# Kernel optimization log

Measured on AMD Instinct MI355X. Metric: run time of the kernel, lower is better.

Reference implementation:

```python
import jax, jax.numpy as jnp
import numpy as np

BITS = 4
IN_F = 4096
OUT_F = 4096
NUMVALS = 200000
TOPX = 10
B, S = 4, 2048


def setup_inputs() -> dict:
    key = jax.random.key(0)
    ks = jax.random.split(key, 9)
    x = jax.random.normal(ks[0], (B, S, IN_F), dtype=jnp.float32)
    qweight = jax.random.randint(ks[1], (IN_F // 32 * BITS, OUT_F),
                                 jnp.iinfo(jnp.int32).min, jnp.iinfo(jnp.int32).max,
                                 dtype=jnp.int32)
    lookup_table = jax.random.normal(ks[2], (OUT_F, 2 ** BITS), dtype=jnp.float32) * 0.02
    bias = jax.random.normal(ks[3], (OUT_F,), dtype=jnp.float32) * 0.01
    rows = jnp.sort(jax.random.randint(ks[4], (OUT_F + 1,), 0, NUMVALS, dtype=jnp.int32))
    rows = rows.at[0].set(0).at[-1].set(NUMVALS)  # valid CSR row pointers
    cols = jax.random.randint(ks[5], (NUMVALS,), 0, IN_F, dtype=jnp.int32)
    vals = jax.random.normal(ks[6], (NUMVALS,), dtype=jnp.float32) * 0.02
    full_rows = jax.random.normal(ks[7], (IN_F, TOPX), dtype=jnp.float32) * 0.02
    full_row_indices = (jnp.arange(TOPX, dtype=jnp.int32) * (OUT_F // TOPX))
    return {"x": x, "qweight": qweight, "lookup_table": lookup_table, "bias": bias,
            "rows": rows, "cols": cols, "vals": vals,
            "full_rows": full_rows, "full_row_indices": full_row_indices}


def _dequant(qweight, lookup_table):
    # unpack 4-bit codes packed along infeatures into each int32 word
    per_word = 32 // BITS
    shifts = (jnp.arange(per_word, dtype=jnp.int32) * BITS)
    codes = (qweight[:, None, :] >> shifts[None, :, None]) & ((1 << BITS) - 1)
    codes = codes.reshape(-1, qweight.shape[1])  # (IN_F, OUT_F)
    # per-output-channel LUT gather: W[i, j] = lut[j, codes[i, j]]
    return jnp.take_along_axis(lookup_table.T, codes, axis=0)  # (IN_F, OUT_F)


def reference(x, qweight, lookup_table, bias, rows, cols, vals, full_rows, full_row_indices):
    w = _dequant(qweight, lookup_table)  # (IN_F, OUT_F) float32
    # CSR sparse outlier correction (row pointers over output channels)
    nnz = vals.shape[0]
    row_ids = jnp.searchsorted(rows, jnp.arange(nnz, dtype=jnp.int32), side="right") - 1
    w = w.at[cols, row_ids].add(vals)
    # topX dense outlier channels
    w = w.at[:, full_row_indices].add(full_rows)
    tokens = x.reshape(-1, x.shape[-1])  # (B*S, IN_F)
    y = tokens @ w + bias
    return y.reshape(x.shape[:-1] + (w.shape[1],))
```

## Files before the change

### kernel.cpp

```cpp
#include <hip/hip_runtime.h>
#include <hip/hip_bf16.h>
#include <stdint.h>

#define IN_F 4096
#define OUT_F 4096
#define MTOK 8192
#define TOPX_N 10
#define NUMVALS 200000

typedef __bf16 bf16x8 __attribute__((ext_vector_type(8)));
typedef float f32x4 __attribute__((ext_vector_type(4)));

__device__ __forceinline__ void gld_lds16(const void* g, void* l) {
    __builtin_amdgcn_global_load_lds((const __attribute__((address_space(1))) void*)g,
                                     (__attribute__((address_space(3))) void*)l, 16, 0, 0);
}

__global__ __launch_bounds__(256) void k_dequant(const int* __restrict__ qw,
                                                 const float* __restrict__ lut,
                                                 __bf16* __restrict__ Wt) {
    __shared__ int qs[64 * 65];
    __shared__ float ls[64 * 16];
    const int b = blockIdx.x;
    const int jc = (b & 63) * 64;
    const int wc = (b >> 6) * 64;
    const int t = threadIdx.x;

    {
        float4 v = *(const float4*)(lut + (size_t)(jc + (t >> 2)) * 16 + (t & 3) * 4);
        *(float4*)(ls + (t >> 2) * 16 + (t & 3) * 4) = v;
    }
#pragma unroll
    for (int p = 0; p < 4; ++p) {
        int idx = t + p * 256;
        int row = idx >> 4;
        int c4 = (idx & 15) * 4;
        int4 v = *(const int4*)(qw + (size_t)(wc + row) * OUT_F + jc + c4);
        int base = row * 65 + c4;
        qs[base] = v.x; qs[base + 1] = v.y; qs[base + 2] = v.z; qs[base + 3] = v.w;
    }
    __syncthreads();

    const int wave = t >> 6, lane = t & 63;
#pragma unroll
    for (int i = 0; i < 16; ++i) {
        const int c = wave * 16 + i;
        const unsigned q = (unsigned)qs[lane * 65 + c];
        const float* lp = ls + c * 16;
        bf16x8 v;
#pragma unroll
        for (int e = 0; e < 8; ++e) v[e] = (__bf16)lp[(q >> (4 * e)) & 15];
        *(bf16x8*)(Wt + (size_t)(jc + c) * IN_F + (size_t)(wc + lane) * 8) = v;
    }
}

__global__ __launch_bounds__(256) void k_csr(const int* __restrict__ rows,
                                             const int* __restrict__ cols,
                                             const float* __restrict__ vals,
                                             __bf16* __restrict__ Wt) {
    int n = blockIdx.x * 256 + threadIdx.x;
    if (n >= NUMVALS) return;
    int lo = 0, hi = OUT_F + 1;
    while (lo < hi) {
        int mid = (lo + hi) >> 1;
        if (rows[mid] <= n) lo = mid + 1; else hi = mid;
    }
    int r = lo - 1;
    int c = cols[n];
    float v = vals[n];
    unsigned* wp = (unsigned*)Wt + (((size_t)r * IN_F + c) >> 1);
    unsigned sh = (c & 1) * 16;
    unsigned old = *wp, assumed;
    do {
        assumed = old;
        union { unsigned u; float f; } cv;
        cv.u = ((assumed >> sh) & 0xFFFFu) << 16;
        __bf16 nb = (__bf16)(cv.f + v);
        unsigned nh = *(unsigned short*)&nb;
        unsigned newv = (assumed & ~(0xFFFFu << sh)) | (nh << sh);
        old = atomicCAS(wp, assumed, newv);
    } while (old != assumed);
}

__global__ void k_topx(const float* __restrict__ fr, const int* __restrict__ fri,
                       __bf16* __restrict__ Wt) {
    int i = blockIdx.x * 256 + threadIdx.x;
    if (i >= IN_F) return;
#pragma unroll
    for (int t = 0; t < TOPX_N; ++t) {
        int j = fri[t];
        __bf16* p = Wt + (size_t)j * IN_F + i;
        *p = (__bf16)((float)*p + fr[(size_t)i * TOPX_N + t]);
    }
}

__global__ void k_cvt(const float* __restrict__ x, __bf16* __restrict__ xb) {
    size_t t = (size_t)blockIdx.x * 256 + threadIdx.x;
    const float4* p = (const float4*)x + 2 * t;
    float4 a = p[0], b = p[1];
    bf16x8 v;
    v[0] = (__bf16)a.x; v[1] = (__bf16)a.y; v[2] = (__bf16)a.z; v[3] = (__bf16)a.w;
    v[4] = (__bf16)b.x; v[5] = (__bf16)b.y; v[6] = (__bf16)b.z; v[7] = (__bf16)b.w;
    ((bf16x8*)xb)[t] = v;
}

#define BK_G 32
#define NKT (IN_F / BK_G)
#define TILE_BYTES 16384

__global__ __launch_bounds__(512, 2) void k_gemm(const __bf16* __restrict__ A,
                                                 const __bf16* __restrict__ Bt,
                                                 const float* __restrict__ bias,
                                                 float* __restrict__ C) {
    __shared__ __align__(1024) char smem[3][2][TILE_BYTES];

    const int tid = threadIdx.x;
    const int wave = tid >> 6, lane = tid & 63;
    const int wm = wave >> 2, wn = wave & 3;

    const int bid = blockIdx.x;
    const int swz = (bid & 7) * 64 + (bid >> 3);
    const int n0 = (swz & 15) * 256;
    const int m0 = (swz >> 4) * 256;

    const int q = lane & 7, g = (lane >> 3) & 3, rh = lane >> 5;
    const int rloc = ((5 * (q - g + 8)) & 7) + 8 * rh;
    const int w0 = wave * 2;

    const char* gA0 = (const char*)(A  + (size_t)(m0 + w0 * 16 + rloc) * IN_F) + g * 16;
    const char* gA1 = gA0 + 16 * IN_F * 2;
    const char* gB0 = (const char*)(Bt + (size_t)(n0 + w0 * 16 + rloc) * IN_F) + g * 16;
    const char* gB1 = gB0 + 16 * IN_F * 2;
    char* lA = (char*)smem[0][0] + w0 * 1024;
    char* lB = (char*)smem[0][1] + w0 * 1024;

    const int lrow = lane & 15, kk = lane >> 4;
    const int rdc = ((5 * lrow + kk) & 7) * 16 + kk * 128 + (lrow >> 3) * 512;
    const int rdA = wm * 8192 + rdc;
    const int rdB = wn * 4096 + rdc;

#define STAGE(boff, koff) do {                               \
        gld_lds16(gA0 + (koff), lA + (boff));                \
        gld_lds16(gA1 + (koff), lA + (boff) + 1024);         \
        gld_lds16(gB0 + (koff), lB + (boff));                \
        gld_lds16(gB1 + (koff), lB + (boff) + 1024);         \
    } while (0)

#define COMPUTE(boff) do {                                                                     \
        const char* pA = (const char*)smem[0][0] + (boff) + rdA;                               \
        const char* pB = (const char*)smem[0][1] + (boff) + rdB;                               \
        bf16x8 bfr[4], af0[4], af1[4];                                                         \
        _Pragma("unroll") for (int n = 0; n < 4; ++n) bfr[n] = *(const bf16x8*)(pB + n * 1024);\
        _Pragma("unroll") for (int m = 0; m < 4; ++m) af0[m] = *(const bf16x8*)(pA + m * 1024);\
        _Pragma("unroll") for (int m = 0; m < 4; ++m) af1[m] = *(const bf16x8*)(pA + 4096 + m * 1024);\
        __builtin_amdgcn_s_setprio(1);                                                         \
        _Pragma("unroll") for (int m = 0; m < 4; ++m)                                          \
            _Pragma("unroll") for (int n = 0; n < 4; ++n)                                      \
                acc[m][n] = __builtin_amdgcn_mfma_f32_16x16x32_bf16(af0[m], bfr[n], acc[m][n], 0, 0, 0); \
        _Pragma("unroll") for (int m = 0; m < 4; ++m)                                          \
            _Pragma("unroll") for (int n = 0; n < 4; ++n)                                      \
                acc[m + 4][n] = __builtin_amdgcn_mfma_f32_16x16x32_bf16(af1[m], bfr[n], acc[m + 4][n], 0, 0, 0); \
        __builtin_amdgcn_s_setprio(0);                                                         \
    } while (0)

    f32x4 acc[8][4] = {};

    STAGE(0, 0);
    STAGE(32768, 64);

    int cboff = 0, sboff = 65536;
    for (int t = 0; t < NKT - 1; ++t) {
        asm volatile("s_waitcnt vmcnt(4)" ::: "memory");
        __builtin_amdgcn_s_barrier();
        asm volatile("" ::: "memory");
        if (t + 2 < NKT) STAGE(sboff, (t + 2) * 64);
        COMPUTE(cboff);
        cboff = cboff == 65536 ? 0 : cboff + 32768;
        sboff = sboff == 65536 ? 0 : sboff + 32768;
    }
    asm volatile("s_waitcnt vmcnt(0)" ::: "memory");
    __builtin_amdgcn_s_barrier();
    asm volatile("" ::: "memory");
    COMPUTE(cboff);

    const int m0w = m0 + wm * 128;
    const int n0w = n0 + wn * 64;
#pragma unroll
    for (int n = 0; n < 4; ++n) {
        const int col = n0w + n * 16 + lrow;
        const float bj = bias[col];
#pragma unroll
        for (int m = 0; m < 8; ++m) {
            const int row = m0w + m * 16 + kk * 4;
#pragma unroll
            for (int r = 0; r < 4; ++r)
                C[(size_t)(row + r) * OUT_F + col] = acc[m][n][r] + bj;
        }
    }
#undef STAGE
#undef COMPUTE
}

extern "C" void kernel_launch(void* const* d_in, const int* in_sizes, int n_in,
                              void* d_out, int out_size, void* d_ws, size_t ws_size,
                              hipStream_t stream) {
    const float* x         = (const float*)d_in[0];
    const int*   qweight   = (const int*)d_in[1];
    const float* lut       = (const float*)d_in[2];
    const float* bias      = (const float*)d_in[3];
    const int*   rows      = (const int*)d_in[4];
    const int*   cols      = (const int*)d_in[5];
    const float* vals      = (const float*)d_in[6];
    const float* full_rows = (const float*)d_in[7];
    const int*   fri       = (const int*)d_in[8];
    float* out = (float*)d_out;

    __bf16* Wt = (__bf16*)d_ws;
    __bf16* xb = (__bf16*)((char*)d_ws + (size_t)OUT_F * IN_F * 2);

    k_dequant<<<dim3(64 * 8), 256, 0, stream>>>(qweight, lut, Wt);
    k_csr<<<dim3((NUMVALS + 255) / 256), 256, 0, stream>>>(rows, cols, vals, Wt);
    k_topx<<<dim3(IN_F / 256), 256, 0, stream>>>(full_rows, fri, Wt);
    k_cvt<<<dim3((size_t)MTOK * IN_F / 8 / 256), 256, 0, stream>>>(x, xb);
    k_gemm<<<dim3((OUT_F / 256) * (MTOK / 256)), 512, 0, stream>>>(xb, Wt, bias, out);
}
```

Before: 536.7 us.

## Restructure GEMM main loop into double-buffered BK=64 with four interleaved MFMA phases

The bf16 GEMM K-step grows from 32 to 64, and the triple-buffered LDS ring becomes a double buffer of 32 KB tiles with a new swizzle. Each K-iteration is split into four quarter phases separated by barriers. Fragment LDS reads and the global-to-LDS staging of the next tiles are interleaved between MFMA bursts. The goal is fewer loop iterations and barriers per FLOP and better overlap of memory traffic with matrix math. The cost is extra barriers per iteration, more register pressure from 2-deep fragments, and staging into the buffer being read, which relies on careful barrier placement.

```diff
diff --git a/kernel.cpp b/kernel.cpp
--- a/kernel.cpp
+++ b/kernel.cpp
@@ -104,84 +104,141 @@
     ((bf16x8*)xb)[t] = v;
 }
 
-#define BK_G 32
+#define BK_G 64
 #define NKT (IN_F / BK_G)
-#define TILE_BYTES 16384
+#define ROWB (IN_F * 2)
+
+#define MFMA_ __builtin_amdgcn_mfma_f32_16x16x32_bf16
 
 __global__ __launch_bounds__(512, 2) void k_gemm(const __bf16* __restrict__ A,
                                                  const __bf16* __restrict__ Bt,
                                                  const float* __restrict__ bias,
                                                  float* __restrict__ C) {
-    __shared__ __align__(1024) char smem[3][2][TILE_BYTES];
+    __shared__ __align__(1024) char smem[2][2][32768];
 
     const int tid = threadIdx.x;
-    const int wave = tid >> 6, lane = tid & 63;
-    const int wm = wave >> 2, wn = wave & 3;
+    const int v = tid >> 6, l = tid & 63;
+    const int wm = v >> 2, wn = v & 3;
 
     const int bid = blockIdx.x;
     const int swz = (bid & 7) * 64 + (bid >> 3);
     const int n0 = (swz & 15) * 256;
     const int m0 = (swz >> 4) * 256;
 
-    const int q = lane & 7, g = (lane >> 3) & 3, rh = lane >> 5;
-    const int rloc = ((5 * (q - g + 8)) & 7) + 8 * rh;
-    const int w0 = wave * 2;
-
-    const char* gA0 = (const char*)(A  + (size_t)(m0 + w0 * 16 + rloc) * IN_F) + g * 16;
-    const char* gA1 = gA0 + 16 * IN_F * 2;
-    const char* gB0 = (const char*)(Bt + (size_t)(n0 + w0 * 16 + rloc) * IN_F) + g * 16;
-    const char* gB1 = gB0 + 16 * IN_F * 2;
-    char* lA = (char*)smem[0][0] + w0 * 1024;
-    char* lB = (char*)smem[0][1] + w0 * 1024;
-
-    const int lrow = lane & 15, kk = lane >> 4;
-    const int rdc = ((5 * lrow + kk) & 7) * 16 + kk * 128 + (lrow >> 3) * 512;
-    const int rdA = wm * 8192 + rdc;
-    const int rdB = wn * 4096 + rdc;
-
-#define STAGE(boff, koff) do {                               \
-        gld_lds16(gA0 + (koff), lA + (boff));                \
-        gld_lds16(gA1 + (koff), lA + (boff) + 1024);         \
-        gld_lds16(gB0 + (koff), lB + (boff));                \
-        gld_lds16(gB1 + (koff), lB + (boff) + 1024);         \
+    const int g = l >> 3;
+    const int r0 = ((l & 7) - g) & 7;
+    const char* pA = (const char*)A  + (size_t)(m0 + 32 * v + r0) * ROWB + g * 16;
+    const char* pB = (const char*)Bt + (size_t)(n0 + 32 * v + r0) * ROWB + g * 16;
+    const int ldA = v * 4096;
+    const int ldB = 32768 + v * 4096;
+
+#define STG(pX, ldX, bo, koff) do {                                              \
+        gld_lds16((pX) + (koff),               (char*)smem + (bo) + (ldX));      \
+        gld_lds16((pX) + (koff) + 8  * ROWB,   (char*)smem + (bo) + (ldX) + 1024);\
+        gld_lds16((pX) + (koff) + 16 * ROWB,   (char*)smem + (bo) + (ldX) + 2048);\
+        gld_lds16((pX) + (koff) + 24 * ROWB,   (char*)smem + (bo) + (ldX) + 3072);\
     } while (0)
 
-#define COMPUTE(boff) do {                                                                     \
-        const char* pA = (const char*)smem[0][0] + (boff) + rdA;                               \
-        const char* pB = (const char*)smem[0][1] + (boff) + rdB;                               \
-        bf16x8 bfr[4], af0[4], af1[4];                                                         \
-        _Pragma("unroll") for (int n = 0; n < 4; ++n) bfr[n] = *(const bf16x8*)(pB + n * 1024);\
-        _Pragma("unroll") for (int m = 0; m < 4; ++m) af0[m] = *(const bf16x8*)(pA + m * 1024);\
-        _Pragma("unroll") for (int m = 0; m < 4; ++m) af1[m] = *(const bf16x8*)(pA + 4096 + m * 1024);\
-        __builtin_amdgcn_s_setprio(1);                                                         \
-        _Pragma("unroll") for (int m = 0; m < 4; ++m)                                          \
-            _Pragma("unroll") for (int n = 0; n < 4; ++n)                                      \
-                acc[m][n] = __builtin_amdgcn_mfma_f32_16x16x32_bf16(af0[m], bfr[n], acc[m][n], 0, 0, 0); \
-        _Pragma("unroll") for (int m = 0; m < 4; ++m)                                          \
-            _Pragma("unroll") for (int n = 0; n < 4; ++n)                                      \
-                acc[m + 4][n] = __builtin_amdgcn_mfma_f32_16x16x32_bf16(af1[m], bfr[n], acc[m + 4][n], 0, 0, 0); \
-        __builtin_amdgcn_s_setprio(0);                                                         \
-    } while (0)
+    const int lrow = l & 15, kk = l >> 4;
+    const int Pb0 = ((lrow + kk) & 7) * 16 + kk * 128 + (lrow >> 3) * 1024;
+    const int Pb1 = ((lrow + kk + 4) & 7) * 16 + (kk + 4) * 128 + (lrow >> 3) * 1024;
+    const int rdA0 = wm * 16384 + Pb0;
+    const int rdA1 = wm * 16384 + Pb1;
+    const int rdB0 = 32768 + wn * 8192 + Pb0;
+    const int rdB1 = 32768 + wn * 8192 + Pb1;
+
+#define FENCE asm volatile("" ::: "memory")
+#define BARRIER do { FENCE; __builtin_amdgcn_s_barrier(); FENCE; } while (0)
 
     f32x4 acc[8][4] = {};
-
-    STAGE(0, 0);
-    STAGE(32768, 64);
-
-    int cboff = 0, sboff = 65536;
-    for (int t = 0; t < NKT - 1; ++t) {
-        asm volatile("s_waitcnt vmcnt(4)" ::: "memory");
+    bf16x8 af[4][2], bfr[4][2];
+
+    STG(pB, ldB, 0, 0);
+    STG(pA, ldA, 0, 0);
+    STG(pB, ldB, 65536, 128);
+    STG(pA, ldA, 65536, 128);
+    asm volatile("s_waitcnt vmcnt(8)" ::: "memory");
+    __builtin_amdgcn_s_barrier();
+    FENCE;
+
+    for (int S = 0; S < NKT; ++S) {
+        const int bo = (S & 1) << 16;
+        const int ko = (S + 2) * 128;
+        const bool stg = (S < NKT - 2);
+
+#pragma unroll
+        for (int n = 0; n < 2; ++n) {
+            bfr[n][0] = *(const bf16x8*)((const char*)smem + bo + rdB0 + n * 2048);
+            bfr[n][1] = *(const bf16x8*)((const char*)smem + bo + rdB1 + n * 2048);
+        }
+#pragma unroll
+        for (int m = 0; m < 4; ++m) {
+            af[m][0] = *(const bf16x8*)((const char*)smem + bo + rdA0 + m * 2048);
+            af[m][1] = *(const bf16x8*)((const char*)smem + bo + rdA1 + m * 2048);
+        }
+        BARRIER;
+        __builtin_amdgcn_s_setprio(1);
+#pragma unroll
+        for (int m = 0; m < 4; ++m)
+#pragma unroll
+            for (int n = 0; n < 2; ++n) {
+                acc[m][n] = MFMA_(af[m][0], bfr[n][0], acc[m][n], 0, 0, 0);
+                acc[m][n] = MFMA_(af[m][1], bfr[n][1], acc[m][n], 0, 0, 0);
+            }
+        __builtin_amdgcn_s_setprio(0);
+        BARRIER;
+
+#pragma unroll
+        for (int n = 2; n < 4; ++n) {
+            bfr[n][0] = *(const bf16x8*)((const char*)smem + bo + rdB0 + n * 2048);
+            bfr[n][1] = *(const bf16x8*)((const char*)smem + bo + rdB1 + n * 2048);
+        }
+        BARRIER;
+        __builtin_amdgcn_s_setprio(1);
+#pragma unroll
+        for (int m = 0; m < 4; ++m)
+#pragma unroll
+            for (int n = 2; n < 4; ++n) {
+                acc[m][n] = MFMA_(af[m][0], bfr[n][0], acc[m][n], 0, 0, 0);
+                acc[m][n] = MFMA_(af[m][1], bfr[n][1], acc[m][n], 0, 0, 0);
+            }
+        __builtin_amdgcn_s_setprio(0);
+        BARRIER;
+
+#pragma unroll
+        for (int m = 0; m < 4; ++m) {
+            af[m][0] = *(const bf16x8*)((const char*)smem + bo + rdA0 + (4 + m) * 2048);
+            af[m][1] = *(const bf16x8*)((const char*)smem + bo + rdA1 + (4 + m) * 2048);
+        }
+        if (stg) STG(pB, ldB, bo, ko);
+        BARRIER;
+        __builtin_amdgcn_s_setprio(1);
+#pragma unroll
+        for (int m = 0; m < 4; ++m)
+#pragma unroll
+            for (int n = 2; n < 4; ++n) {
+                acc[4 + m][n] = MFMA_(af[m][0], bfr[n][0], acc[4 + m][n], 0, 0, 0);
+                acc[4 + m][n] = MFMA_(af[m][1], bfr[n][1], acc[4 + m][n], 0, 0, 0);
+            }
+        __builtin_amdgcn_s_setprio(0);
+        BARRIER;
+
+        if (stg) STG(pA, ldA, bo, ko);
+        BARRIER;
+        __builtin_amdgcn_s_setprio(1);
+#pragma unroll
+        for (int m = 0; m < 4; ++m)
+#pragma unroll
+            for (int n = 0; n < 2; ++n) {
+                acc[4 + m][n] = MFMA_(af[m][0], bfr[n][0], acc[4 + m][n], 0, 0, 0);
+                acc[4 + m][n] = MFMA_(af[m][1], bfr[n][1], acc[4 + m][n], 0, 0, 0);
+            }
+        __builtin_amdgcn_s_setprio(0);
+        if (stg) { asm volatile("s_waitcnt vmcnt(8)" ::: "memory"); }
+        else     { asm volatile("s_waitcnt vmcnt(0)" ::: "memory"); }
         __builtin_amdgcn_s_barrier();
-        asm volatile("" ::: "memory");
-        if (t + 2 < NKT) STAGE(sboff, (t + 2) * 64);
-        COMPUTE(cboff);
-        cboff = cboff == 65536 ? 0 : cboff + 32768;
-        sboff = sboff == 65536 ? 0 : sboff + 32768;
-    }
-    asm volatile("s_waitcnt vmcnt(0)" ::: "memory");
-    __builtin_amdgcn_s_barrier();
-    asm volatile("" ::: "memory");
-    COMPUTE(cboff);
+        FENCE;
+    }
 
     const int m0w = m0 + wm * 128;
     const int n0w = n0 + wn * 64;
@@ -197,8 +254,9 @@
                 C[(size_t)(row + r) * OUT_F + col] = acc[m][n][r] + bj;
         }
     }
-#undef STAGE
-#undef COMPUTE
+#undef STG
+#undef FENCE
+#undef BARRIER
 }
 
 extern "C" void kernel_launch(void* const* d_in, const int* in_sizes, int n_in,
```

After: 546.1 us. About the same (+1.8%).

## Fuse CSR and topX fixups into one kernel; restructure GEMM into paired-tile windows

Applied to the files above, without the earlier changes.

Merges the CSR outlier and topX dense-column correction kernels into a single launch, with topX now using the atomic CAS add so it can run concurrently with the CSR updates. The GEMM main loop changes from a 3-stage ring with one barrier per K-tile to a 4-buffer scheme that stages two tiles, computes two, and synchronises with a full vmcnt(0) wait. This halves the barrier count. The trade-off is that loads are no longer overlapped at single-tile granularity, and each wait drains all outstanding loads.

```diff
diff --git a/kernel.cpp b/kernel.cpp
--- a/kernel.cpp
+++ b/kernel.cpp
@@ -7,6 +7,7 @@
 #define MTOK 8192
 #define TOPX_N 10
 #define NUMVALS 200000
+#define CSR_BLOCKS ((NUMVALS + 255) / 256)
 
 typedef __bf16 bf16x8 __attribute__((ext_vector_type(8)));
 typedef float f32x4 __attribute__((ext_vector_type(4)));
@@ -54,22 +55,9 @@
     }
 }
 
-__global__ __launch_bounds__(256) void k_csr(const int* __restrict__ rows,
-                                             const int* __restrict__ cols,
-                                             const float* __restrict__ vals,
-                                             __bf16* __restrict__ Wt) {
-    int n = blockIdx.x * 256 + threadIdx.x;
-    if (n >= NUMVALS) return;
-    int lo = 0, hi = OUT_F + 1;
-    while (lo < hi) {
-        int mid = (lo + hi) >> 1;
-        if (rows[mid] <= n) lo = mid + 1; else hi = mid;
-    }
-    int r = lo - 1;
-    int c = cols[n];
-    float v = vals[n];
-    unsigned* wp = (unsigned*)Wt + (((size_t)r * IN_F + c) >> 1);
-    unsigned sh = (c & 1) * 16;
+__device__ __forceinline__ void bf16_cas_add(__bf16* Wt, size_t elem, float v) {
+    unsigned* wp = (unsigned*)Wt + (elem >> 1);
+    unsigned sh = (unsigned)(elem & 1) * 16;
     unsigned old = *wp, assumed;
     do {
         assumed = old;
@@ -77,20 +65,36 @@
         cv.u = ((assumed >> sh) & 0xFFFFu) << 16;
         __bf16 nb = (__bf16)(cv.f + v);
         unsigned nh = *(unsigned short*)&nb;
-        unsigned newv = (assumed & ~(0xFFFFu << sh)) | (nh << sh);
+        unsigned newv = (assumed & ~(0xFFFFu << sh)) | ((unsigned)nh << sh);
         old = atomicCAS(wp, assumed, newv);
     } while (old != assumed);
 }
 
-__global__ void k_topx(const float* __restrict__ fr, const int* __restrict__ fri,
-                       __bf16* __restrict__ Wt) {
-    int i = blockIdx.x * 256 + threadIdx.x;
-    if (i >= IN_F) return;
-#pragma unroll
-    for (int t = 0; t < TOPX_N; ++t) {
-        int j = fri[t];
-        __bf16* p = Wt + (size_t)j * IN_F + i;
-        *p = (__bf16)((float)*p + fr[(size_t)i * TOPX_N + t]);
+__global__ __launch_bounds__(256) void k_fix(const int* __restrict__ rows,
+                                             const int* __restrict__ cols,
+                                             const float* __restrict__ vals,
+                                             const float* __restrict__ fr,
+                                             const int* __restrict__ fri,
+                                             __bf16* __restrict__ Wt) {
+    const int b = blockIdx.x;
+    if (b < CSR_BLOCKS) {
+        int n = b * 256 + threadIdx.x;
+        if (n >= NUMVALS) return;
+        int lo = 0, hi = OUT_F + 1;
+        while (lo < hi) {
+            int mid = (lo + hi) >> 1;
+            if (rows[mid] <= n) lo = mid + 1; else hi = mid;
+        }
+        int r = lo - 1;
+        bf16_cas_add(Wt, (size_t)r * IN_F + cols[n], vals[n]);
+    } else {
+        int i = (b - CSR_BLOCKS) * 256 + threadIdx.x;
+        if (i >= IN_F) return;
+#pragma unroll
+        for (int t = 0; t < TOPX_N; ++t) {
+            int j = fri[t];
+            bf16_cas_add(Wt, (size_t)j * IN_F + i, fr[(size_t)i * TOPX_N + t]);
+        }
     }
 }
 
@@ -104,84 +108,84 @@
     ((bf16x8*)xb)[t] = v;
 }
 
-#define BK_G 32
-#define NKT (IN_F / BK_G)
-#define TILE_BYTES 16384
+#define ROWB (IN_F * 2)
+#define MFMA_ __builtin_amdgcn_mfma_f32_16x16x32_bf16
 
 __global__ __launch_bounds__(512, 2) void k_gemm(const __bf16* __restrict__ A,
                                                  const __bf16* __restrict__ Bt,
                                                  const float* __restrict__ bias,
                                                  float* __restrict__ C) {
-    __shared__ __align__(1024) char smem[3][2][TILE_BYTES];
+    __shared__ __align__(1024) char smem[4][32768];
 
     const int tid = threadIdx.x;
-    const int wave = tid >> 6, lane = tid & 63;
-    const int wm = wave >> 2, wn = wave & 3;
+    const int wv = tid >> 6, l = tid & 63;
+    const int wm = wv >> 2, wn = wv & 3;
 
     const int bid = blockIdx.x;
     const int swz = (bid & 7) * 64 + (bid >> 3);
     const int n0 = (swz & 15) * 256;
     const int m0 = (swz >> 4) * 256;
 
-    const int q = lane & 7, g = (lane >> 3) & 3, rh = lane >> 5;
-    const int rloc = ((5 * (q - g + 8)) & 7) + 8 * rh;
-    const int w0 = wave * 2;
-
-    const char* gA0 = (const char*)(A  + (size_t)(m0 + w0 * 16 + rloc) * IN_F) + g * 16;
-    const char* gA1 = gA0 + 16 * IN_F * 2;
-    const char* gB0 = (const char*)(Bt + (size_t)(n0 + w0 * 16 + rloc) * IN_F) + g * 16;
-    const char* gB1 = gB0 + 16 * IN_F * 2;
-    char* lA = (char*)smem[0][0] + w0 * 1024;
-    char* lB = (char*)smem[0][1] + w0 * 1024;
-
-    const int lrow = lane & 15, kk = lane >> 4;
+    const int q = l & 7, gq = (l >> 3) & 3, rh = l >> 5;
+    const int rloc = ((5 * (q - gq + 8)) & 7) + 8 * rh;
+    const char* gA  = (const char*)A  + (size_t)(m0 + wv * 32 + rloc) * ROWB + gq * 16;
+    const char* gB  = (const char*)Bt + (size_t)(n0 + wv * 32 + rloc) * ROWB + gq * 16;
+    const char* gA2 = gA + 16 * ROWB;
+    const char* gB2 = gB + 16 * ROWB;
+    const int lo = wv * 2048 + l * 16;
+
+#define STAGE_TILE(bi, koff) do {                                   \
+        gld_lds16(gA  + (koff), (char*)smem[bi] + lo);              \
+        gld_lds16(gA2 + (koff), (char*)smem[bi] + lo + 1024);       \
+        gld_lds16(gB  + (koff), (char*)smem[bi] + 16384 + lo);      \
+        gld_lds16(gB2 + (koff), (char*)smem[bi] + 16384 + lo + 1024);\
+    } while (0)
+
+    const int lrow = l & 15, kk = l >> 4;
     const int rdc = ((5 * lrow + kk) & 7) * 16 + kk * 128 + (lrow >> 3) * 512;
     const int rdA = wm * 8192 + rdc;
-    const int rdB = wn * 4096 + rdc;
-
-#define STAGE(boff, koff) do {                               \
-        gld_lds16(gA0 + (koff), lA + (boff));                \
-        gld_lds16(gA1 + (koff), lA + (boff) + 1024);         \
-        gld_lds16(gB0 + (koff), lB + (boff));                \
-        gld_lds16(gB1 + (koff), lB + (boff) + 1024);         \
+    const int rdB = 16384 + wn * 4096 + rdc;
+
+    f32x4 acc[8][4] = {};
+
+#define COMPUTE(bi) do {                                                         \
+        bf16x8 bfr[4], af[8];                                                    \
+        _Pragma("unroll") for (int n = 0; n < 4; ++n)                            \
+            bfr[n] = *(const bf16x8*)((const char*)smem[bi] + rdB + n * 1024);   \
+        _Pragma("unroll") for (int m = 0; m < 8; ++m)                            \
+            af[m] = *(const bf16x8*)((const char*)smem[bi] + rdA + m * 1024);    \
+        __builtin_amdgcn_s_setprio(1);                                           \
+        _Pragma("unroll") for (int m = 0; m < 8; ++m)                            \
+            _Pragma("unroll") for (int n = 0; n < 4; ++n)                        \
+                acc[m][n] = MFMA_(af[m], bfr[n], acc[m][n], 0, 0, 0);            \
+        __builtin_amdgcn_s_setprio(0);                                           \
     } while (0)
 
-#define COMPUTE(boff) do {                                                                     \
-        const char* pA = (const char*)smem[0][0] + (boff) + rdA;                               \
-        const char* pB = (const char*)smem[0][1] + (boff) + rdB;                               \
-        bf16x8 bfr[4], af0[4], af1[4];                                                         \
-        _Pragma("unroll") for (int n = 0; n < 4; ++n) bfr[n] = *(const bf16x8*)(pB + n * 1024);\
-        _Pragma("unroll") for (int m = 0; m < 4; ++m) af0[m] = *(const bf16x8*)(pA + m * 1024);\
-        _Pragma("unroll") for (int m = 0; m < 4; ++m) af1[m] = *(const bf16x8*)(pA + 4096 + m * 1024);\
-        __builtin_amdgcn_s_setprio(1);                                                         \
-        _Pragma("unroll") for (int m = 0; m < 4; ++m)                                          \
-            _Pragma("unroll") for (int n = 0; n < 4; ++n)                                      \
-                acc[m][n] = __builtin_amdgcn_mfma_f32_16x16x32_bf16(af0[m], bfr[n], acc[m][n], 0, 0, 0); \
-        _Pragma("unroll") for (int m = 0; m < 4; ++m)                                          \
-            _Pragma("unroll") for (int n = 0; n < 4; ++n)                                      \
-                acc[m + 4][n] = __builtin_amdgcn_mfma_f32_16x16x32_bf16(af1[m], bfr[n], acc[m + 4][n], 0, 0, 0); \
-        __builtin_amdgcn_s_setprio(0);                                                         \
+#define WINSYNC do {                                      \
+        asm volatile("s_waitcnt vmcnt(0)" ::: "memory");  \
+        __builtin_amdgcn_s_barrier();                     \
+        asm volatile("" ::: "memory");                    \
     } while (0)
 
-    f32x4 acc[8][4] = {};
-
-    STAGE(0, 0);
-    STAGE(32768, 64);
-
-    int cboff = 0, sboff = 65536;
-    for (int t = 0; t < NKT - 1; ++t) {
-        asm volatile("s_waitcnt vmcnt(4)" ::: "memory");
-        __builtin_amdgcn_s_barrier();
-        asm volatile("" ::: "memory");
-        if (t + 2 < NKT) STAGE(sboff, (t + 2) * 64);
-        COMPUTE(cboff);
-        cboff = cboff == 65536 ? 0 : cboff + 32768;
-        sboff = sboff == 65536 ? 0 : sboff + 32768;
-    }
-    asm volatile("s_waitcnt vmcnt(0)" ::: "memory");
-    __builtin_amdgcn_s_barrier();
-    asm volatile("" ::: "memory");
-    COMPUTE(cboff);
+    STAGE_TILE(0, 0);
+    STAGE_TILE(1, 64);
+    WINSYNC;
+
+    for (int h = 0; h < 32; ++h) {
+        STAGE_TILE(2, 128);
+        STAGE_TILE(3, 192);
+        COMPUTE(0);
+        COMPUTE(1);
+        WINSYNC;
+        if (h < 31) {
+            STAGE_TILE(0, 256);
+            STAGE_TILE(1, 320);
+        }
+        COMPUTE(2);
+        COMPUTE(3);
+        WINSYNC;
+        gA += 256; gA2 += 256; gB += 256; gB2 += 256;
+    }
 
     const int m0w = m0 + wm * 128;
     const int n0w = n0 + wn * 64;
@@ -197,8 +201,9 @@
                 C[(size_t)(row + r) * OUT_F + col] = acc[m][n][r] + bj;
         }
     }
-#undef STAGE
+#undef STAGE_TILE
 #undef COMPUTE
+#undef WINSYNC
 }
 
 extern "C" void kernel_launch(void* const* d_in, const int* in_sizes, int n_in,
@@ -219,8 +224,7 @@
     __bf16* xb = (__bf16*)((char*)d_ws + (size_t)OUT_F * IN_F * 2);
 
     k_dequant<<<dim3(64 * 8), 256, 0, stream>>>(qweight, lut, Wt);
-    k_csr<<<dim3((NUMVALS + 255) / 256), 256, 0, stream>>>(rows, cols, vals, Wt);
-    k_topx<<<dim3(IN_F / 256), 256, 0, stream>>>(full_rows, fri, Wt);
+    k_fix<<<dim3(CSR_BLOCKS + IN_F / 256), 256, 0, stream>>>(rows, cols, vals, full_rows, fri, Wt);
     k_cvt<<<dim3((size_t)MTOK * IN_F / 8 / 256), 256, 0, stream>>>(x, xb);
     k_gemm<<<dim3((OUT_F / 256) * (MTOK / 256)), 512, 0, stream>>>(xb, Wt, bias, out);
 }
```

Measured after the change: 577.2 us. 1.08x slower.
